# Optimization experiments

Hardware: AMD Instinct MI355X
Metric: run time of the kernel (lower is better)

Reference implementation:

```python
import jax, jax.numpy as jnp
import numpy as np
import math

SR = 48000
HOP = 480
NH = 6
MEL_CH = 128
CHUNK = 256


def _lin_interp(x, out_len):
    # torch F.interpolate(mode='linear', align_corners=False) along last axis
    T = x.shape[-1]
    scale = T / out_len
    pos = (jnp.arange(out_len, dtype=jnp.float32) + 0.5) * scale - 0.5
    pos = jnp.clip(pos, 0.0, T - 1)
    i0 = jnp.floor(pos).astype(jnp.int32)
    i1 = jnp.minimum(i0 + 1, T - 1)
    w = (pos - i0.astype(jnp.float32))
    return x[..., i0] * (1.0 - w) + x[..., i1] * w


def _conv1d(x, w, b, pad):
    y = jax.lax.conv_general_dilated(x, w, (1,), [(pad, pad)],
                                     dimension_numbers=('NCH', 'OIH', 'NCH'))
    return y + b[None, :, None]


def _wrapped_cumsum(x, chunk=CHUNK):
    # faithful chunked phase-wrap cumsum: carry_{i+1} = fmod(total_i + carry_i, 1)
    B, C, T = x.shape
    n = T // chunk
    xc = x.reshape(B, C, n, chunk)
    cum = jnp.cumsum(xc, axis=-1)            # per-chunk cumsum [B,C,n,chunk]
    totals = jnp.moveaxis(cum[..., -1], -1, 0)  # [n,B,C]

    def step(carry, t):
        new = jnp.fmod(carry + t, 1.0)
        return new, carry  # emit carry *before* this chunk

    carry0 = jnp.zeros((B, C), dtype=x.dtype)
    _, carries = jax.lax.scan(step, carry0, totals)
    carries = jnp.moveaxis(carries, 0, -1)   # [B,C,n]
    out = jnp.fmod(cum + carries[..., None], 1.0)
    return out.reshape(B, C, T)


def setup_inputs() -> dict:
    key = jax.random.key(0)
    ks = jax.random.split(key, 10)
    B, T = 4, 2000
    T_AUD = T * HOP
    f0 = jax.random.uniform(ks[0], (B, T), jnp.float32, 0.0, 500.0)
    mel = jax.random.normal(ks[1], (B, MEL_CH, T), jnp.float32)
    noise = jax.random.normal(ks[2], (B, 1, T_AUD), jnp.float32)
    conv1_w = jax.random.normal(ks[3], (32, 1 + MEL_CH, 5), jnp.float32) * 0.05
    conv1_b = jax.random.normal(ks[4], (32,), jnp.float32) * 0.05
    conv2_w = jax.random.normal(ks[5], (NH, 32, 1), jnp.float32) * 0.05
    conv2_b = jax.random.normal(ks[6], (NH,), jnp.float32) * 0.05
    amp_logscale = -jnp.log(jnp.arange(1, NH + 1, dtype=jnp.float32))
    phase_offset = jax.random.normal(ks[7], (NH,), jnp.float32) * 0.1
    log_noise_voiced = jnp.asarray(math.log(0.003), jnp.float32)
    log_noise_unvoiced = jnp.asarray(math.log(0.003), jnp.float32)
    return dict(f0=f0, mel=mel, noise=noise, conv1_w=conv1_w, conv1_b=conv1_b,
                conv2_w=conv2_w, conv2_b=conv2_b, amp_logscale=amp_logscale,
                phase_offset=phase_offset, log_noise_voiced=log_noise_voiced,
                log_noise_unvoiced=log_noise_unvoiced)


def reference(f0, mel, noise, conv1_w, conv1_b, conv2_w, conv2_b,
              amp_logscale, phase_offset, log_noise_voiced, log_noise_unvoiced):
    f0 = f0[:, None, :]                                   # [B,1,T]
    T = f0.shape[-1]
    k = jnp.arange(1, NH + 1, dtype=jnp.float32)[None, :, None]

    # mel+f0 conditioned amplitude predictor (mel already at f0 frame rate)
    h = _conv1d(jnp.concatenate([f0, mel], axis=1), conv1_w, conv1_b, pad=2)
    amp_mod = _conv1d(jax.nn.silu(h), conv2_w, conv2_b, pad=0)  # [B,NH,T]

    T_aud = T * HOP
    f0_up = _lin_interp(f0, T_aud)                        # [B,1,T_aud]
    phase_inc = f0_up / SR
    base_phase = _wrapped_cumsum(phase_inc) * (2.0 * math.pi)

    offset = phase_offset[None, :, None]
    harmonics = jnp.sin(k * base_phase + offset * (2.0 * math.pi))
    harmonics = harmonics * jnp.exp(amp_logscale)[None, :, None]

    amp_mod_up = _lin_interp(amp_mod, T_aud)
    harmonics = harmonics * (2.0 * jax.nn.sigmoid(amp_mod_up))

    nyquist = SR / 2.0
    voiced_mask = (f0_up > 1.0).astype(jnp.float32)
    aa_mask = jax.nn.sigmoid((nyquist - k * f0_up) / (nyquist * 0.05))
    harmonics = harmonics * (aa_mask * voiced_mask)

    noise_amp = voiced_mask * jnp.exp(log_noise_voiced) + \
                (1.0 - voiced_mask) * jnp.exp(log_noise_unvoiced)
    noise_out = noise * noise_amp
    return jnp.concatenate([harmonics, noise_out], axis=1)  # [B,NH+1,T_aud]
```

## Files before the change

kernel.cpp:

```cpp
#include <hip/hip_runtime.h>
#include <math.h>

#define NH      6
#define T_IN    2000
#define T_AUD   960000
#define CHUNK   256
#define NCHUNK  3750
#define NB      4
#define C_IN    129
#define C_MID   32
#define CSPLIT  3
#define NC_PER  43
#define SPLIT_STRIDE (NB * C_MID * T_IN)

__device__ __forceinline__ double f0up_at(const float* __restrict__ f0b, int t) {
    double pos = ((double)t + 0.5) * (1.0 / 480.0) - 0.5;
    pos = pos < 0.0 ? 0.0 : (pos > 1999.0 ? 1999.0 : pos);
    int i0 = (int)pos;
    int i1 = i0 + 1; if (i1 > 1999) i1 = 1999;
    double w = pos - (double)i0;
    return (double)f0b[i0] * (1.0 - w) + (double)f0b[i1] * w;
}

__global__ void k_conv1(const float* __restrict__ f0, const float* __restrict__ mel,
                        const float* __restrict__ w1, float* __restrict__ hpart) {
    const int t0  = blockIdx.x * 256;
    const int b   = blockIdx.y >> 2;
    const int o0  = (blockIdx.y & 3) * 8;
    const int z   = blockIdx.z;
    const int cbase = z * NC_PER;
    const int tid = threadIdx.x;

    __shared__ float xl[NC_PER][264];

    for (int idx = tid; idx < NC_PER * 66; idx += 256) {
        const int r = idx / 66;
        const int j = idx - r * 66;
        const int c = cbase + r;
        const float* row = (c == 0) ? (f0 + b * T_IN)
                                    : (mel + ((size_t)(b * 128 + (c - 1))) * T_IN);
        const int gt = t0 - 4 + j * 4;
        float4 v;
        if (gt >= 0 && gt + 3 < T_IN) {
            v = *(const float4*)(row + gt);
        } else {
            v.x = (gt + 0 >= 0 && gt + 0 < T_IN) ? row[gt + 0] : 0.0f;
            v.y = (gt + 1 >= 0 && gt + 1 < T_IN) ? row[gt + 1] : 0.0f;
            v.z = (gt + 2 >= 0 && gt + 2 < T_IN) ? row[gt + 2] : 0.0f;
            v.w = (gt + 3 >= 0 && gt + 3 < T_IN) ? row[gt + 3] : 0.0f;
        }
        *(float4*)(&xl[r][j * 4]) = v;
    }
    __syncthreads();

    float acc[8];
    #pragma unroll
    for (int oo = 0; oo < 8; ++oo) acc[oo] = 0.0f;

    for (int c = 0; c < NC_PER; ++c) {
        const float x0 = xl[c][tid + 2];
        const float x1 = xl[c][tid + 3];
        const float x2 = xl[c][tid + 4];
        const float x3 = xl[c][tid + 5];
        const float x4 = xl[c][tid + 6];
        const int cg = cbase + c;
        #pragma unroll
        for (int oo = 0; oo < 8; ++oo) {
            const float* wp = w1 + (size_t)(o0 + oo) * (C_IN * 5) + cg * 5;
            acc[oo] = fmaf(wp[0], x0, acc[oo]);
            acc[oo] = fmaf(wp[1], x1, acc[oo]);
            acc[oo] = fmaf(wp[2], x2, acc[oo]);
            acc[oo] = fmaf(wp[3], x3, acc[oo]);
            acc[oo] = fmaf(wp[4], x4, acc[oo]);
        }
    }

    const int t = t0 + tid;
    if (t < T_IN) {
        #pragma unroll
        for (int oo = 0; oo < 8; ++oo)
            hpart[(size_t)z * SPLIT_STRIDE + ((size_t)(b * C_MID + o0 + oo)) * T_IN + t] = acc[oo];
    }
}

__global__ void k_conv2(const float* __restrict__ hpart, const float* __restrict__ b1,
                        const float* __restrict__ w2, const float* __restrict__ b2,
                        float* __restrict__ amp) {
    const int g = blockIdx.x * 256 + threadIdx.x;
    if (g >= NB * NH * T_IN) return;
    const int b = g / (NH * T_IN);
    const int r = g - b * (NH * T_IN);
    const int h = r / T_IN;
    const int t = r - h * T_IN;
    float acc = b2[h];
    #pragma unroll
    for (int o = 0; o < C_MID; ++o) {
        const size_t base = ((size_t)(b * C_MID + o)) * T_IN + t;
        float v = hpart[base] + hpart[SPLIT_STRIDE + base] + hpart[2 * SPLIT_STRIDE + base] + b1[o];
        const float sg = __builtin_amdgcn_rcpf(1.0f + __expf(-v));
        acc = fmaf(w2[h * C_MID + o], v * sg, acc);
    }
    amp[g] = acc;
}

__global__ void k_totals(const float* __restrict__ f0, double* __restrict__ totals) {
    const int b    = blockIdx.y;
    const int lane = threadIdx.x & 63;
    const int wid  = threadIdx.x >> 6;
    const int chunk = blockIdx.x * 4 + wid;
    if (chunk >= NCHUNK) return;
    const float* f0b = f0 + b * T_IN;
    const int t0 = chunk * CHUNK + lane * 4;
    double s = 0.0;
    #pragma unroll
    for (int j = 0; j < 4; ++j) s += f0up_at(f0b, t0 + j);
    s *= (1.0 / 48000.0);
    #pragma unroll
    for (int d = 32; d >= 1; d >>= 1) s += __shfl_down(s, d, 64);
    if (lane == 0) totals[b * NCHUNK + chunk] = s;
}

__global__ void k_carries(const double* __restrict__ totals, double* __restrict__ carries) {
    const int b   = blockIdx.x;
    const int tid = threadIdx.x;
    const double* tb = totals + b * NCHUNK;
    double* cb = carries + b * NCHUNK;
    const int base = tid * 15;
    double psum = 0.0;
    for (int j = 0; j < 15; ++j) {
        const int n = base + j;
        if (n < NCHUNK) psum += tb[n];
    }
    __shared__ double part[256];
    part[tid] = psum;
    __syncthreads();
    double run = psum;
    for (int d = 1; d < 256; d <<= 1) {
        const double tadd = (tid >= d) ? part[tid - d] : 0.0;
        __syncthreads();
        run += tadd;
        part[tid] = run;
        __syncthreads();
    }
    double S = run - psum;
    for (int j = 0; j < 15; ++j) {
        const int n = base + j;
        if (n < NCHUNK) {
            cb[n] = S - floor(S);
            S += tb[n];
        }
    }
}

__global__ void k_main(const float* __restrict__ f0, const float* __restrict__ noise,
                       const float* __restrict__ amp, const double* __restrict__ carries,
                       const float* __restrict__ amp_logscale, const float* __restrict__ phase_offset,
                       const float* __restrict__ lnv, const float* __restrict__ lnu,
                       float* __restrict__ out) {
    const int b    = blockIdx.y;
    const int tid  = threadIdx.x;
    const int lane = tid & 63;
    const int wid  = tid >> 6;
    const int chunk = blockIdx.x * 4 + wid;
    if (chunk >= NCHUNK) return;

    const float* f0b = f0 + b * T_IN;
    const int t0 = chunk * CHUNK + lane * 4;

    double f0u[4], inc[4];
    #pragma unroll
    for (int j = 0; j < 4; ++j) {
        f0u[j] = f0up_at(f0b, t0 + j);
        inc[j] = f0u[j] * (1.0 / 48000.0);
    }
    const double loc = inc[0] + inc[1] + inc[2] + inc[3];

    double v = loc;
    #pragma unroll
    for (int d = 1; d < 64; d <<= 1) {
        const double n = __shfl_up(v, d, 64);
        if (lane >= d) v += n;
    }
    double run = v - loc + carries[b * NCHUNK + chunk];

    float ph[4], f0f[4], voiced[4], wgt[4];
    int i0[4], i1[4];
    #pragma unroll
    for (int j = 0; j < 4; ++j) {
        run += inc[j];
        ph[j]  = (float)(run - floor(run));
        f0f[j] = (float)f0u[j];
        voiced[j] = (f0f[j] > 1.0f) ? 1.0f : 0.0f;
        double posd = ((double)(t0 + j) + 0.5) * (1.0 / 480.0) - 0.5;
        posd = posd < 0.0 ? 0.0 : (posd > 1999.0 ? 1999.0 : posd);
        i0[j] = (int)posd;
        i1[j] = (i0[j] + 1 > 1999) ? 1999 : i0[j] + 1;
        wgt[j] = (float)(posd - (double)i0[j]);
    }

    const size_t outb = (size_t)b * 7 * T_AUD;
    #pragma unroll
    for (int h = 0; h < NH; ++h) {
        const float kf = (float)(h + 1);
        const float ascale = __expf(amp_logscale[h]);
        const float off = phase_offset[h];
        const float* ab = amp + ((size_t)(b * NH + h)) * T_IN;
        float4 res;
        float r[4];
        #pragma unroll
        for (int j = 0; j < 4; ++j) {
            const float am  = ab[i0[j]] * (1.0f - wgt[j]) + ab[i1[j]] * wgt[j];
            const float sig = __builtin_amdgcn_rcpf(1.0f + __expf(-am));
            const float arg = kf * ph[j] + off;
            const float fr  = arg - floorf(arg);
            const float sn  = __builtin_amdgcn_sinf(fr);
            const float aa  = __builtin_amdgcn_rcpf(1.0f + __expf(-(24000.0f - kf * f0f[j]) * (1.0f / 1200.0f)));
            r[j] = sn * ascale * (2.0f * sig) * (aa * voiced[j]);
        }
        res.x = r[0]; res.y = r[1]; res.z = r[2]; res.w = r[3];
        *(float4*)(out + outb + (size_t)h * T_AUD + t0) = res;
    }

    const float nv = __expf(lnv[0]);
    const float nu = __expf(lnu[0]);
    const float4 nz = *(const float4*)(noise + (size_t)b * T_AUD + t0);
    float4 no;
    no.x = nz.x * (voiced[0] > 0.0f ? nv : nu);
    no.y = nz.y * (voiced[1] > 0.0f ? nv : nu);
    no.z = nz.z * (voiced[2] > 0.0f ? nv : nu);
    no.w = nz.w * (voiced[3] > 0.0f ? nv : nu);
    *(float4*)(out + outb + (size_t)6 * T_AUD + t0) = no;
}

extern "C" void kernel_launch(void* const* d_in, const int* in_sizes, int n_in,
                              void* d_out, int out_size, void* d_ws, size_t ws_size,
                              hipStream_t stream) {
    const float* f0   = (const float*)d_in[0];
    const float* mel  = (const float*)d_in[1];
    const float* nois = (const float*)d_in[2];
    const float* w1   = (const float*)d_in[3];
    const float* b1   = (const float*)d_in[4];
    const float* w2   = (const float*)d_in[5];
    const float* b2   = (const float*)d_in[6];
    const float* alog = (const float*)d_in[7];
    const float* poff = (const float*)d_in[8];
    const float* lnv  = (const float*)d_in[9];
    const float* lnu  = (const float*)d_in[10];
    float* out = (float*)d_out;

    float*  hpart   = (float*)d_ws;
    float*  amp     = (float*)((char*)d_ws + 3072000);
    double* totals  = (double*)((char*)d_ws + 3264000);
    double* carries = (double*)((char*)d_ws + 3384000);

    k_conv1<<<dim3(8, 16, CSPLIT), 256, 0, stream>>>(f0, mel, w1, hpart);
    k_conv2<<<dim3((NB * NH * T_IN + 255) / 256), 256, 0, stream>>>(hpart, b1, w2, b2, amp);
    k_totals<<<dim3((NCHUNK + 3) / 4, NB), 256, 0, stream>>>(f0, totals);
    k_carries<<<dim3(NB), 256, 0, stream>>>(totals, carries);
    k_main<<<dim3((NCHUNK + 3) / 4, NB), 256, 0, stream>>>(f0, nois, amp, carries,
                                                           alog, poff, lnv, lnu, out);
}
```

Measured before the change: 201.0 us.

## Replace chunked audio-rate phase scan with closed-form per-frame prefix, fuse conv layers

Phase accumulation is now computed analytically. A small per-frame prefix sum over f0 (in double) is combined with a closed-form quadratic term for the linearly interpolated segment, which removes the per-sample totals kernel, the carry scan and the in-wave shuffle scan. The two conv layers are fused into one kernel that keeps the SiLU hidden activations in shared memory, so the partial-sum buffer round trip disappears. The main kernel also takes a fast path when all four samples share one interpolation frame. This cuts five launches to three, but it relies on the closed-form phase matching the original chunked fmod accumulation closely enough, with large absolute phase values held in double.

```diff
diff --git a/kernel.cpp b/kernel.cpp
--- a/kernel.cpp
+++ b/kernel.cpp
@@ -4,137 +4,107 @@
 #define NH      6
 #define T_IN    2000
 #define T_AUD   960000
-#define CHUNK   256
-#define NCHUNK  3750
 #define NB      4
 #define C_IN    129
 #define C_MID   32
-#define CSPLIT  3
-#define NC_PER  43
-#define SPLIT_STRIDE (NB * C_MID * T_IN)
-
-__device__ __forceinline__ double f0up_at(const float* __restrict__ f0b, int t) {
-    double pos = ((double)t + 0.5) * (1.0 / 480.0) - 0.5;
-    pos = pos < 0.0 ? 0.0 : (pos > 1999.0 ? 1999.0 : pos);
-    int i0 = (int)pos;
-    int i1 = i0 + 1; if (i1 > 1999) i1 = 1999;
-    double w = pos - (double)i0;
-    return (double)f0b[i0] * (1.0 - w) + (double)f0b[i1] * w;
-}
-
-__global__ void k_conv1(const float* __restrict__ f0, const float* __restrict__ mel,
-                        const float* __restrict__ w1, float* __restrict__ hpart) {
-    const int t0  = blockIdx.x * 256;
-    const int b   = blockIdx.y >> 2;
-    const int o0  = (blockIdx.y & 3) * 8;
-    const int z   = blockIdx.z;
-    const int cbase = z * NC_PER;
+
+__global__ __launch_bounds__(512) void k_amp(const float* __restrict__ f0,
+                                             const float* __restrict__ mel,
+                                             const float* __restrict__ w1,
+                                             const float* __restrict__ b1,
+                                             const float* __restrict__ w2,
+                                             const float* __restrict__ b2,
+                                             float* __restrict__ amp) {
+    const int b   = blockIdx.y;
+    const int t0  = blockIdx.x * 64;
     const int tid = threadIdx.x;
-
-    __shared__ float xl[NC_PER][264];
-
-    for (int idx = tid; idx < NC_PER * 66; idx += 256) {
-        const int r = idx / 66;
-        const int j = idx - r * 66;
-        const int c = cbase + r;
-        const float* row = (c == 0) ? (f0 + b * T_IN)
-                                    : (mel + ((size_t)(b * 128 + (c - 1))) * T_IN);
-        const int gt = t0 - 4 + j * 4;
-        float4 v;
-        if (gt >= 0 && gt + 3 < T_IN) {
-            v = *(const float4*)(row + gt);
-        } else {
-            v.x = (gt + 0 >= 0 && gt + 0 < T_IN) ? row[gt + 0] : 0.0f;
-            v.y = (gt + 1 >= 0 && gt + 1 < T_IN) ? row[gt + 1] : 0.0f;
-            v.z = (gt + 2 >= 0 && gt + 2 < T_IN) ? row[gt + 2] : 0.0f;
-            v.w = (gt + 3 >= 0 && gt + 3 < T_IN) ? row[gt + 3] : 0.0f;
-        }
-        *(float4*)(&xl[r][j * 4]) = v;
+    const int tt    = tid & 63;
+    const int layer = tid >> 6;
+    const int o0    = layer * 4;
+
+    __shared__ float xl[16][72];
+    __shared__ float hsil[C_MID][64];
+
+    float acc[4] = {0.f, 0.f, 0.f, 0.f};
+
+    for (int cg = 0; cg < C_IN; cg += 16) {
+        const int ng = (C_IN - cg) < 16 ? (C_IN - cg) : 16;
+        __syncthreads();
+        for (int idx = tid; idx < ng * 18; idx += 512) {
+            const int r = idx / 18;
+            const int j = idx - r * 18;
+            const int c = cg + r;
+            const float* row = (c == 0) ? (f0 + b * T_IN)
+                                        : (mel + ((size_t)(b * 128 + (c - 1))) * T_IN);
+            const int gt = t0 - 4 + j * 4;
+            float4 v;
+            if (gt >= 0 && gt + 3 < T_IN) {
+                v = *(const float4*)(row + gt);
+            } else {
+                v.x = (gt + 0 >= 0 && gt + 0 < T_IN) ? row[gt + 0] : 0.0f;
+                v.y = (gt + 1 >= 0 && gt + 1 < T_IN) ? row[gt + 1] : 0.0f;
+                v.z = (gt + 2 >= 0 && gt + 2 < T_IN) ? row[gt + 2] : 0.0f;
+                v.w = (gt + 3 >= 0 && gt + 3 < T_IN) ? row[gt + 3] : 0.0f;
+            }
+            *(float4*)(&xl[r][j * 4]) = v;
+        }
+        __syncthreads();
+        for (int ci = 0; ci < ng; ++ci) {
+            const float x0 = xl[ci][tt + 2];
+            const float x1 = xl[ci][tt + 3];
+            const float x2 = xl[ci][tt + 4];
+            const float x3 = xl[ci][tt + 5];
+            const float x4 = xl[ci][tt + 6];
+            const int cgl = cg + ci;
+            #pragma unroll
+            for (int oo = 0; oo < 4; ++oo) {
+                const float* wp = w1 + (size_t)(o0 + oo) * (C_IN * 5) + cgl * 5;
+                acc[oo] = fmaf(wp[0], x0, acc[oo]);
+                acc[oo] = fmaf(wp[1], x1, acc[oo]);
+                acc[oo] = fmaf(wp[2], x2, acc[oo]);
+                acc[oo] = fmaf(wp[3], x3, acc[oo]);
+                acc[oo] = fmaf(wp[4], x4, acc[oo]);
+            }
+        }
+    }
+
+    #pragma unroll
+    for (int oo = 0; oo < 4; ++oo) {
+        const float v = acc[oo] + b1[o0 + oo];
+        hsil[o0 + oo][tt] = v * __builtin_amdgcn_rcpf(1.0f + __expf(-v));
     }
     __syncthreads();
 
-    float acc[8];
-    #pragma unroll
-    for (int oo = 0; oo < 8; ++oo) acc[oo] = 0.0f;
-
-    for (int c = 0; c < NC_PER; ++c) {
-        const float x0 = xl[c][tid + 2];
-        const float x1 = xl[c][tid + 3];
-        const float x2 = xl[c][tid + 4];
-        const float x3 = xl[c][tid + 5];
-        const float x4 = xl[c][tid + 6];
-        const int cg = cbase + c;
-        #pragma unroll
-        for (int oo = 0; oo < 8; ++oo) {
-            const float* wp = w1 + (size_t)(o0 + oo) * (C_IN * 5) + cg * 5;
-            acc[oo] = fmaf(wp[0], x0, acc[oo]);
-            acc[oo] = fmaf(wp[1], x1, acc[oo]);
-            acc[oo] = fmaf(wp[2], x2, acc[oo]);
-            acc[oo] = fmaf(wp[3], x3, acc[oo]);
-            acc[oo] = fmaf(wp[4], x4, acc[oo]);
-        }
-    }
-
-    const int t = t0 + tid;
-    if (t < T_IN) {
-        #pragma unroll
-        for (int oo = 0; oo < 8; ++oo)
-            hpart[(size_t)z * SPLIT_STRIDE + ((size_t)(b * C_MID + o0 + oo)) * T_IN + t] = acc[oo];
-    }
-}
-
-__global__ void k_conv2(const float* __restrict__ hpart, const float* __restrict__ b1,
-                        const float* __restrict__ w2, const float* __restrict__ b2,
-                        float* __restrict__ amp) {
-    const int g = blockIdx.x * 256 + threadIdx.x;
-    if (g >= NB * NH * T_IN) return;
-    const int b = g / (NH * T_IN);
-    const int r = g - b * (NH * T_IN);
-    const int h = r / T_IN;
-    const int t = r - h * T_IN;
-    float acc = b2[h];
-    #pragma unroll
-    for (int o = 0; o < C_MID; ++o) {
-        const size_t base = ((size_t)(b * C_MID + o)) * T_IN + t;
-        float v = hpart[base] + hpart[SPLIT_STRIDE + base] + hpart[2 * SPLIT_STRIDE + base] + b1[o];
-        const float sg = __builtin_amdgcn_rcpf(1.0f + __expf(-v));
-        acc = fmaf(w2[h * C_MID + o], v * sg, acc);
-    }
-    amp[g] = acc;
-}
-
-__global__ void k_totals(const float* __restrict__ f0, double* __restrict__ totals) {
-    const int b    = blockIdx.y;
-    const int lane = threadIdx.x & 63;
-    const int wid  = threadIdx.x >> 6;
-    const int chunk = blockIdx.x * 4 + wid;
-    if (chunk >= NCHUNK) return;
-    const float* f0b = f0 + b * T_IN;
-    const int t0 = chunk * CHUNK + lane * 4;
-    double s = 0.0;
-    #pragma unroll
-    for (int j = 0; j < 4; ++j) s += f0up_at(f0b, t0 + j);
-    s *= (1.0 / 48000.0);
-    #pragma unroll
-    for (int d = 32; d >= 1; d >>= 1) s += __shfl_down(s, d, 64);
-    if (lane == 0) totals[b * NCHUNK + chunk] = s;
-}
-
-__global__ void k_carries(const double* __restrict__ totals, double* __restrict__ carries) {
+    if (tid < NH * 64) {
+        const int h = tid >> 6;
+        const int t = tid & 63;
+        float a = b2[h];
+        #pragma unroll
+        for (int o = 0; o < C_MID; ++o)
+            a = fmaf(w2[h * C_MID + o], hsil[o][t], a);
+        const int gt = t0 + t;
+        if (gt < T_IN) amp[((size_t)(b * NH + h)) * T_IN + gt] = a;
+    }
+}
+
+__global__ void k_prefix(const float* __restrict__ f0, double* __restrict__ P) {
     const int b   = blockIdx.x;
     const int tid = threadIdx.x;
-    const double* tb = totals + b * NCHUNK;
-    double* cb = carries + b * NCHUNK;
-    const int base = tid * 15;
-    double psum = 0.0;
-    for (int j = 0; j < 15; ++j) {
-        const int n = base + j;
-        if (n < NCHUNK) psum += tb[n];
+    const float* f0b = f0 + b * T_IN;
+
+    double loc[8];
+    double c = 0.0;
+    const int base = tid * 8;
+    #pragma unroll
+    for (int j = 0; j < 8; ++j) {
+        const int idx = base + j;
+        loc[j] = c;
+        if (idx < T_IN - 1) c += (double)f0b[idx] + (double)f0b[idx + 1];
     }
     __shared__ double part[256];
-    part[tid] = psum;
+    part[tid] = c;
     __syncthreads();
-    double run = psum;
+    double run = c;
     for (int d = 1; d < 256; d <<= 1) {
         const double tadd = (tid >= d) ? part[tid - d] : 0.0;
         __syncthreads();
@@ -142,60 +112,71 @@
         part[tid] = run;
         __syncthreads();
     }
-    double S = run - psum;
-    for (int j = 0; j < 15; ++j) {
-        const int n = base + j;
-        if (n < NCHUNK) {
-            cb[n] = S - floor(S);
-            S += tb[n];
-        }
+    const double excl  = run - c;
+    const double base0 = 240.0 * (double)f0b[0];
+    #pragma unroll
+    for (int j = 0; j < 8; ++j) {
+        const int idx = base + j;
+        if (idx < T_IN) P[b * T_IN + idx] = base0 + 240.0 * (excl + loc[j]);
     }
 }
 
 __global__ void k_main(const float* __restrict__ f0, const float* __restrict__ noise,
-                       const float* __restrict__ amp, const double* __restrict__ carries,
+                       const float* __restrict__ amp, const double* __restrict__ P,
                        const float* __restrict__ amp_logscale, const float* __restrict__ phase_offset,
                        const float* __restrict__ lnv, const float* __restrict__ lnu,
                        float* __restrict__ out) {
-    const int b    = blockIdx.y;
-    const int tid  = threadIdx.x;
-    const int lane = tid & 63;
-    const int wid  = tid >> 6;
-    const int chunk = blockIdx.x * 4 + wid;
-    if (chunk >= NCHUNK) return;
-
-    const float* f0b = f0 + b * T_IN;
-    const int t0 = chunk * CHUNK + lane * 4;
-
-    double f0u[4], inc[4];
+    const int b  = blockIdx.y;
+    const int g  = blockIdx.x * 256 + threadIdx.x;
+    const int t0 = g * 4;
+    if (t0 >= T_AUD) return;
+
+    const float*  f0b = f0 + b * T_IN;
+    const double* Pb  = P + b * T_IN;
+
+    int iv[4], mv[4];
     #pragma unroll
     for (int j = 0; j < 4; ++j) {
-        f0u[j] = f0up_at(f0b, t0 + j);
-        inc[j] = f0u[j] * (1.0 / 48000.0);
-    }
-    const double loc = inc[0] + inc[1] + inc[2] + inc[3];
-
-    double v = loc;
-    #pragma unroll
-    for (int d = 1; d < 64; d <<= 1) {
-        const double n = __shfl_up(v, d, 64);
-        if (lane >= d) v += n;
-    }
-    double run = v - loc + carries[b * NCHUNK + chunk];
-
-    float ph[4], f0f[4], voiced[4], wgt[4];
-    int i0[4], i1[4];
+        const int t = t0 + j;
+        int u = t - 240; if (u < 0) u = 0;
+        int i = u / 480; if (i > 1998) i = 1998;
+        iv[j] = i;
+        mv[j] = t - i * 480 - 240;
+    }
+    const bool uni = (iv[0] == iv[3]);
+
+    double Pi[4]; float fa[4], fd[4];
+    if (uni) {
+        const double p = Pb[iv[0]];
+        const float  a = f0b[iv[0]];
+        const float  d = f0b[iv[0] + 1] - a;
+        #pragma unroll
+        for (int j = 0; j < 4; ++j) { Pi[j] = p; fa[j] = a; fd[j] = d; }
+    } else {
+        #pragma unroll
+        for (int j = 0; j < 4; ++j) {
+            Pi[j] = Pb[iv[j]];
+            fa[j] = f0b[iv[j]];
+            fd[j] = f0b[iv[j] + 1] - fa[j];
+        }
+    }
+
+    float ph[4], w[4], f0f[4], voiced[4];
     #pragma unroll
     for (int j = 0; j < 4; ++j) {
-        run += inc[j];
-        ph[j]  = (float)(run - floor(run));
-        f0f[j] = (float)f0u[j];
+        const int n = mv[j] + 1;
+        const double dn = (double)n;
+        const double Wn = (n <= 0) ? 0.0 : ((n <= 480) ? dn * dn * (1.0 / 960.0) : dn - 240.0);
+        const double E  = Pi[j] + dn * (double)fa[j] + (double)fd[j] * Wn;
+        const double phase = E * (1.0 / 48000.0);
+        ph[j] = (float)(phase - floor(phase));
+
+        double wd = ((double)mv[j] + 0.5) * (1.0 / 480.0);
+        wd = wd < 0.0 ? 0.0 : (wd > 1.0 ? 1.0 : wd);
+        w[j] = (float)wd;
+        const double f0u = (double)fa[j] + (double)fd[j] * wd;
+        f0f[j] = (float)f0u;
         voiced[j] = (f0f[j] > 1.0f) ? 1.0f : 0.0f;
-        double posd = ((double)(t0 + j) + 0.5) * (1.0 / 480.0) - 0.5;
-        posd = posd < 0.0 ? 0.0 : (posd > 1999.0 ? 1999.0 : posd);
-        i0[j] = (int)posd;
-        i1[j] = (i0[j] + 1 > 1999) ? 1999 : i0[j] + 1;
-        wgt[j] = (float)(posd - (double)i0[j]);
     }
 
     const size_t outb = (size_t)b * 7 * T_AUD;
@@ -205,19 +186,31 @@
         const float ascale = __expf(amp_logscale[h]);
         const float off = phase_offset[h];
         const float* ab = amp + ((size_t)(b * NH + h)) * T_IN;
-        float4 res;
+
+        float am[4];
+        if (uni) {
+            const float a0 = ab[iv[0]];
+            const float dd = ab[iv[0] + 1] - a0;
+            #pragma unroll
+            for (int j = 0; j < 4; ++j) am[j] = fmaf(dd, w[j], a0);
+        } else {
+            #pragma unroll
+            for (int j = 0; j < 4; ++j)
+                am[j] = fmaf(ab[iv[j] + 1] - ab[iv[j]], w[j], ab[iv[j]]);
+        }
+
         float r[4];
         #pragma unroll
         for (int j = 0; j < 4; ++j) {
-            const float am  = ab[i0[j]] * (1.0f - wgt[j]) + ab[i1[j]] * wgt[j];
-            const float sig = __builtin_amdgcn_rcpf(1.0f + __expf(-am));
+            const float sig = __builtin_amdgcn_rcpf(1.0f + __expf(-am[j]));
             const float arg = kf * ph[j] + off;
             const float fr  = arg - floorf(arg);
             const float sn  = __builtin_amdgcn_sinf(fr);
-            const float aa  = __builtin_amdgcn_rcpf(1.0f + __expf(-(24000.0f - kf * f0f[j]) * (1.0f / 1200.0f)));
+            const float aa  = __builtin_amdgcn_rcpf(
+                1.0f + __expf(-(24000.0f - kf * f0f[j]) * (1.0f / 1200.0f)));
             r[j] = sn * ascale * (2.0f * sig) * (aa * voiced[j]);
         }
-        res.x = r[0]; res.y = r[1]; res.z = r[2]; res.w = r[3];
+        float4 res; res.x = r[0]; res.y = r[1]; res.z = r[2]; res.w = r[3];
         *(float4*)(out + outb + (size_t)h * T_AUD + t0) = res;
     }
 
@@ -248,15 +241,11 @@
     const float* lnu  = (const float*)d_in[10];
     float* out = (float*)d_out;
 
-    float*  hpart   = (float*)d_ws;
-    float*  amp     = (float*)((char*)d_ws + 3072000);
-    double* totals  = (double*)((char*)d_ws + 3264000);
-    double* carries = (double*)((char*)d_ws + 3384000);
-
-    k_conv1<<<dim3(8, 16, CSPLIT), 256, 0, stream>>>(f0, mel, w1, hpart);
-    k_conv2<<<dim3((NB * NH * T_IN + 255) / 256), 256, 0, stream>>>(hpart, b1, w2, b2, amp);
-    k_totals<<<dim3((NCHUNK + 3) / 4, NB), 256, 0, stream>>>(f0, totals);
-    k_carries<<<dim3(NB), 256, 0, stream>>>(totals, carries);
-    k_main<<<dim3((NCHUNK + 3) / 4, NB), 256, 0, stream>>>(f0, nois, amp, carries,
-                                                           alog, poff, lnv, lnu, out);
-}
+    float*  amp = (float*)d_ws;
+    double* P   = (double*)((char*)d_ws + 192000);
+
+    k_amp<<<dim3(32, NB), 512, 0, stream>>>(f0, mel, w1, b1, w2, b2, amp);
+    k_prefix<<<dim3(NB), 256, 0, stream>>>(f0, P);
+    k_main<<<dim3((T_AUD / 4 + 255) / 256, NB), 256, 0, stream>>>(
+        f0, nois, amp, P, alog, poff, lnv, lnu, out);
+}
```

New measurement: 206.6 us. 2.8% more time.

## Replace chunked audio-rate phase scan with closed-form per-frame prefix sums

Applied to the files above, without the earlier changes.

The phase cumsum over the upsampled f0 is rewritten analytically: a single small kernel computes a per-frame prefix of the piecewise-linear f0 integral, and the main kernel evaluates the phase at each sample in closed form from that prefix plus a quadratic term. This removes the totals kernel, the carries scan, the per-wave double-precision shuffle scan and most fp64 work in the main kernel. The main kernel also stages its few needed f0, prefix and amp values plus constants in shared memory per block. The cost is that phase is now computed in float from a fractional prefix, which can differ slightly from the reference's chunked fmod cumsum.

```diff
diff --git a/kernel.cpp b/kernel.cpp
--- a/kernel.cpp
+++ b/kernel.cpp
@@ -4,23 +4,12 @@
 #define NH      6
 #define T_IN    2000
 #define T_AUD   960000
-#define CHUNK   256
-#define NCHUNK  3750
 #define NB      4
 #define C_IN    129
 #define C_MID   32
 #define CSPLIT  3
 #define NC_PER  43
 #define SPLIT_STRIDE (NB * C_MID * T_IN)
-
-__device__ __forceinline__ double f0up_at(const float* __restrict__ f0b, int t) {
-    double pos = ((double)t + 0.5) * (1.0 / 480.0) - 0.5;
-    pos = pos < 0.0 ? 0.0 : (pos > 1999.0 ? 1999.0 : pos);
-    int i0 = (int)pos;
-    int i1 = i0 + 1; if (i1 > 1999) i1 = 1999;
-    double w = pos - (double)i0;
-    return (double)f0b[i0] * (1.0 - w) + (double)f0b[i1] * w;
-}
 
 __global__ void k_conv1(const float* __restrict__ f0, const float* __restrict__ mel,
                         const float* __restrict__ w1, float* __restrict__ hpart) {
@@ -103,38 +92,24 @@
     amp[g] = acc;
 }
 
-__global__ void k_totals(const float* __restrict__ f0, double* __restrict__ totals) {
-    const int b    = blockIdx.y;
-    const int lane = threadIdx.x & 63;
-    const int wid  = threadIdx.x >> 6;
-    const int chunk = blockIdx.x * 4 + wid;
-    if (chunk >= NCHUNK) return;
-    const float* f0b = f0 + b * T_IN;
-    const int t0 = chunk * CHUNK + lane * 4;
-    double s = 0.0;
-    #pragma unroll
-    for (int j = 0; j < 4; ++j) s += f0up_at(f0b, t0 + j);
-    s *= (1.0 / 48000.0);
-    #pragma unroll
-    for (int d = 32; d >= 1; d >>= 1) s += __shfl_down(s, d, 64);
-    if (lane == 0) totals[b * NCHUNK + chunk] = s;
-}
-
-__global__ void k_carries(const double* __restrict__ totals, double* __restrict__ carries) {
+__global__ void k_prefix(const float* __restrict__ f0, float* __restrict__ Pf) {
     const int b   = blockIdx.x;
     const int tid = threadIdx.x;
-    const double* tb = totals + b * NCHUNK;
-    double* cb = carries + b * NCHUNK;
-    const int base = tid * 15;
-    double psum = 0.0;
-    for (int j = 0; j < 15; ++j) {
-        const int n = base + j;
-        if (n < NCHUNK) psum += tb[n];
+    const float* f0b = f0 + b * T_IN;
+
+    double loc[8];
+    double c = 0.0;
+    const int base = tid * 8;
+    #pragma unroll
+    for (int j = 0; j < 8; ++j) {
+        const int idx = base + j;
+        loc[j] = c;
+        if (idx < T_IN - 1) c += (double)f0b[idx] + (double)f0b[idx + 1];
     }
     __shared__ double part[256];
-    part[tid] = psum;
+    part[tid] = c;
     __syncthreads();
-    double run = psum;
+    double run = c;
     for (int d = 1; d < 256; d <<= 1) {
         const double tadd = (tid >= d) ? part[tid - d] : 0.0;
         __syncthreads();
@@ -142,93 +117,121 @@
         part[tid] = run;
         __syncthreads();
     }
-    double S = run - psum;
-    for (int j = 0; j < 15; ++j) {
-        const int n = base + j;
-        if (n < NCHUNK) {
-            cb[n] = S - floor(S);
-            S += tb[n];
-        }
-    }
-}
-
-__global__ void k_main(const float* __restrict__ f0, const float* __restrict__ noise,
-                       const float* __restrict__ amp, const double* __restrict__ carries,
-                       const float* __restrict__ amp_logscale, const float* __restrict__ phase_offset,
-                       const float* __restrict__ lnv, const float* __restrict__ lnu,
-                       float* __restrict__ out) {
-    const int b    = blockIdx.y;
-    const int tid  = threadIdx.x;
-    const int lane = tid & 63;
-    const int wid  = tid >> 6;
-    const int chunk = blockIdx.x * 4 + wid;
-    if (chunk >= NCHUNK) return;
+    const double excl  = run - c;
+    const double base0 = 240.0 * (double)f0b[0];
+    #pragma unroll
+    for (int j = 0; j < 8; ++j) {
+        const int idx = base + j;
+        if (idx < T_IN) {
+            const double P = (base0 + 240.0 * (excl + loc[j])) * (1.0 / 48000.0);
+            Pf[b * T_IN + idx] = (float)(P - floor(P));
+        }
+    }
+}
+
+__global__ __launch_bounds__(256) void k_main(
+        const float* __restrict__ f0, const float* __restrict__ noise,
+        const float* __restrict__ amp, const float* __restrict__ Pf,
+        const float* __restrict__ amp_logscale, const float* __restrict__ phase_offset,
+        const float* __restrict__ lnv, const float* __restrict__ lnu,
+        float* __restrict__ out) {
+    const int b   = blockIdx.y;
+    const int tid = threadIdx.x;
+    const int s0  = blockIdx.x * 1024;
+    const int t0  = s0 + tid * 4;
+
+    __shared__ float sf0[6];
+    __shared__ float sPf[4];
+    __shared__ float sam[NH][5];
+    __shared__ float sasc[NH], soff[NH], snv, snu;
+
+    const int ulo  = (s0 - 240) < 0 ? 0 : (s0 - 240);
+    int i_lo = (unsigned)ulo / 480u;
+    if (i_lo > 1998) i_lo = 1998;
 
     const float* f0b = f0 + b * T_IN;
-    const int t0 = chunk * CHUNK + lane * 4;
-
-    double f0u[4], inc[4];
+    const float* Pfb = Pf + b * T_IN;
+
+    if (tid < 6) {
+        int idx = i_lo + tid; if (idx > 1999) idx = 1999;
+        sf0[tid] = f0b[idx];
+    } else if (tid >= 8 && tid < 12) {
+        int idx = i_lo + (tid - 8); if (idx > 1999) idx = 1999;
+        sPf[tid - 8] = Pfb[idx];
+    } else if (tid >= 16 && tid < 46) {
+        const int h  = (tid - 16) / 5;
+        const int jj = (tid - 16) - h * 5;
+        int idx = i_lo + jj; if (idx > 1999) idx = 1999;
+        sam[h][jj] = amp[((size_t)(b * NH + h)) * T_IN + idx];
+    } else if (tid >= 48 && tid < 54) {
+        sasc[tid - 48] = __expf(amp_logscale[tid - 48]);
+    } else if (tid >= 56 && tid < 62) {
+        soff[tid - 56] = phase_offset[tid - 56];
+    } else if (tid == 62) {
+        snv = __expf(lnv[0]);
+    } else if (tid == 63) {
+        snu = __expf(lnu[0]);
+    }
+    __syncthreads();
+
+    if (t0 >= T_AUD) return;
+
+    const float inv48k = 1.0f / 48000.0f;
+    float ph[4], wd[4], f0f[4], voiced[4];
+    int li[4];
     #pragma unroll
     for (int j = 0; j < 4; ++j) {
-        f0u[j] = f0up_at(f0b, t0 + j);
-        inc[j] = f0u[j] * (1.0 / 48000.0);
-    }
-    const double loc = inc[0] + inc[1] + inc[2] + inc[3];
-
-    double v = loc;
-    #pragma unroll
-    for (int d = 1; d < 64; d <<= 1) {
-        const double n = __shfl_up(v, d, 64);
-        if (lane >= d) v += n;
-    }
-    double run = v - loc + carries[b * NCHUNK + chunk];
-
-    float ph[4], f0f[4], voiced[4], wgt[4];
-    int i0[4], i1[4];
-    #pragma unroll
-    for (int j = 0; j < 4; ++j) {
-        run += inc[j];
-        ph[j]  = (float)(run - floor(run));
-        f0f[j] = (float)f0u[j];
+        const int t = t0 + j;
+        const int u = (t - 240) < 0 ? 0 : (t - 240);
+        int i = (unsigned)u / 480u;
+        if (i > 1998) i = 1998;
+        li[j] = i - i_lo;
+        const int m = t - i * 480 - 240;
+        const int n = m + 1;
+        const float nf = (float)n;
+        const float Wn = (n <= 0) ? 0.0f
+                       : ((n <= 480) ? nf * nf * (1.0f / 960.0f) : nf - 240.0f);
+        const float fa = sf0[li[j]];
+        const float fd = sf0[li[j] + 1] - fa;
+        const float pr = sPf[li[j]] + (nf * fa + fd * Wn) * inv48k;
+        ph[j] = pr - floorf(pr);
+
+        float w = ((float)m + 0.5f) * (1.0f / 480.0f);
+        w = w < 0.0f ? 0.0f : (w > 1.0f ? 1.0f : w);
+        wd[j] = w;
+        f0f[j] = fmaf(fd, w, fa);
         voiced[j] = (f0f[j] > 1.0f) ? 1.0f : 0.0f;
-        double posd = ((double)(t0 + j) + 0.5) * (1.0 / 480.0) - 0.5;
-        posd = posd < 0.0 ? 0.0 : (posd > 1999.0 ? 1999.0 : posd);
-        i0[j] = (int)posd;
-        i1[j] = (i0[j] + 1 > 1999) ? 1999 : i0[j] + 1;
-        wgt[j] = (float)(posd - (double)i0[j]);
     }
 
     const size_t outb = (size_t)b * 7 * T_AUD;
     #pragma unroll
     for (int h = 0; h < NH; ++h) {
         const float kf = (float)(h + 1);
-        const float ascale = __expf(amp_logscale[h]);
-        const float off = phase_offset[h];
-        const float* ab = amp + ((size_t)(b * NH + h)) * T_IN;
-        float4 res;
+        const float ascale = sasc[h];
+        const float off = soff[h];
         float r[4];
         #pragma unroll
         for (int j = 0; j < 4; ++j) {
-            const float am  = ab[i0[j]] * (1.0f - wgt[j]) + ab[i1[j]] * wgt[j];
+            const float a0 = sam[h][li[j]];
+            const float am = fmaf(sam[h][li[j] + 1] - a0, wd[j], a0);
             const float sig = __builtin_amdgcn_rcpf(1.0f + __expf(-am));
             const float arg = kf * ph[j] + off;
             const float fr  = arg - floorf(arg);
             const float sn  = __builtin_amdgcn_sinf(fr);
-            const float aa  = __builtin_amdgcn_rcpf(1.0f + __expf(-(24000.0f - kf * f0f[j]) * (1.0f / 1200.0f)));
+            const float aa  = __builtin_amdgcn_rcpf(
+                1.0f + __expf(-(24000.0f - kf * f0f[j]) * (1.0f / 1200.0f)));
             r[j] = sn * ascale * (2.0f * sig) * (aa * voiced[j]);
         }
-        res.x = r[0]; res.y = r[1]; res.z = r[2]; res.w = r[3];
+        float4 res; res.x = r[0]; res.y = r[1]; res.z = r[2]; res.w = r[3];
         *(float4*)(out + outb + (size_t)h * T_AUD + t0) = res;
     }
 
-    const float nv = __expf(lnv[0]);
-    const float nu = __expf(lnu[0]);
     const float4 nz = *(const float4*)(noise + (size_t)b * T_AUD + t0);
     float4 no;
-    no.x = nz.x * (voiced[0] > 0.0f ? nv : nu);
-    no.y = nz.y * (voiced[1] > 0.0f ? nv : nu);
-    no.z = nz.z * (voiced[2] > 0.0f ? nv : nu);
-    no.w = nz.w * (voiced[3] > 0.0f ? nv : nu);
+    no.x = nz.x * (voiced[0] > 0.0f ? snv : snu);
+    no.y = nz.y * (voiced[1] > 0.0f ? snv : snu);
+    no.z = nz.z * (voiced[2] > 0.0f ? snv : snu);
+    no.w = nz.w * (voiced[3] > 0.0f ? snv : snu);
     *(float4*)(out + outb + (size_t)6 * T_AUD + t0) = no;
 }
 
@@ -248,15 +251,13 @@
     const float* lnu  = (const float*)d_in[10];
     float* out = (float*)d_out;
 
-    float*  hpart   = (float*)d_ws;
-    float*  amp     = (float*)((char*)d_ws + 3072000);
-    double* totals  = (double*)((char*)d_ws + 3264000);
-    double* carries = (double*)((char*)d_ws + 3384000);
+    float* hpart = (float*)d_ws;
+    float* amp   = (float*)((char*)d_ws + 3072000);
+    float* Pfrac = (float*)((char*)d_ws + 3264000);
 
     k_conv1<<<dim3(8, 16, CSPLIT), 256, 0, stream>>>(f0, mel, w1, hpart);
     k_conv2<<<dim3((NB * NH * T_IN + 255) / 256), 256, 0, stream>>>(hpart, b1, w2, b2, amp);
-    k_totals<<<dim3((NCHUNK + 3) / 4, NB), 256, 0, stream>>>(f0, totals);
-    k_carries<<<dim3(NB), 256, 0, stream>>>(totals, carries);
-    k_main<<<dim3((NCHUNK + 3) / 4, NB), 256, 0, stream>>>(f0, nois, amp, carries,
-                                                           alog, poff, lnv, lnu, out);
-}
+    k_prefix<<<dim3(NB), 256, 0, stream>>>(f0, Pfrac);
+    k_main<<<dim3((T_AUD + 1023) / 1024, NB), 256, 0, stream>>>(
+        f0, nois, amp, Pfrac, alog, poff, lnv, lnu, out);
+}
```

New measurement: 190.8 us. 5.1% less time.
